# Kernel tuning notes

Hardware: AMD Instinct MI355X
Metric: run time of the kernel (lower is better)

Reference implementation:

```python
import jax, jax.numpy as jnp
import numpy as np

G, NPG, D_IN, HID, NH, DH = 128, 256, 15, 128, 8, 16
N = G * NPG
E = 1_048_576
NLAYERS = 3
EPS = 1e-5


def ln(x, g, b):
    m = x.mean(-1, keepdims=True)
    v = ((x - m) ** 2).mean(-1, keepdims=True)
    return (x - m) * jax.lax.rsqrt(v + EPS) * g + b


def gcn_conv(x, src, dst, W, b):
    # PyG GCNConv: add self-loops, symmetric deg^-1/2 normalization
    n = x.shape[0]
    h = x @ W  # [N, H]
    loop = jnp.arange(n)
    s = jnp.concatenate([src, loop])
    d = jnp.concatenate([dst, loop])
    deg = jnp.zeros((n,), x.dtype).at[d].add(1.0)  # >=1 due to self-loops
    dis = jax.lax.rsqrt(deg)
    coef = (dis[s] * dis[d])[:, None]
    return jnp.zeros_like(h).at[d].add(h[s] * coef) + b


def setup_inputs() -> dict:
    key = jax.random.key(0)
    ks = jax.random.split(key, 40)
    i = iter(range(40))

    def w(shape, scale=0.05):
        return jax.random.normal(ks[next(i)], shape, jnp.float32) * scale

    inp = {
        'x': jax.random.normal(ks[next(i)], (N, D_IN), jnp.float32),
        'edge_index': jax.random.randint(ks[next(i)], (2, E), 0, N),
        'batch': jnp.repeat(jnp.arange(G), NPG),  # 128 graphs x 256 nodes
        # input_proj: Linear + LayerNorm
        'W_in': w((D_IN, HID)), 'b_in': jnp.zeros((HID,)),
        'g_in': jnp.ones((HID,)), 'be_in': jnp.zeros((HID,)),
        # 3 GCNConv layers + LayerNorms (stacked)
        'Wc': w((NLAYERS, HID, HID)), 'bc': jnp.zeros((NLAYERS, HID)),
        'gn': jnp.ones((NLAYERS, HID)), 'bn': jnp.zeros((NLAYERS, HID)),
        # MultiheadAttention (in_proj split into q/k/v) + out_proj + post-LN
        'Wq': w((HID, HID)), 'bq': jnp.zeros((HID,)),
        'Wk': w((HID, HID)), 'bk': jnp.zeros((HID,)),
        'Wv': w((HID, HID)), 'bv': jnp.zeros((HID,)),
        'Wo': w((HID, HID)), 'bo': jnp.zeros((HID,)),
        'ga': jnp.ones((HID,)), 'ba': jnp.zeros((HID,)),
        # classifier: Linear(3H->H)+LN, Linear(H->H//2), Linear(H//2->2)
        'W1': w((3 * HID, HID)), 'b1': jnp.zeros((HID,)),
        'g1': jnp.ones((HID,)), 'beta1': jnp.zeros((HID,)),
        'W2': w((HID, HID // 2)), 'b2': jnp.zeros((HID // 2,)),
        'W3': w((HID // 2, 2)), 'b3': jnp.zeros((2,)),
    }
    return inp


def reference(x, edge_index, batch, W_in, b_in, g_in, be_in, Wc, bc, gn, bn,
              Wq, bq, Wk, bk, Wv, bv, Wo, bo, ga, ba,
              W1, b1, g1, beta1, W2, b2, W3, b3):
    src, dst = edge_index[0], edge_index[1]
    # input_proj (dropout is identity in eval)
    h = jax.nn.relu(ln(x @ W_in + b_in, g_in, be_in))
    # causal_graph_forward: GCN + LN + ReLU, residual for layers > 0
    for i in range(NLAYERS):
        h_res = h
        h = jax.nn.relu(ln(gcn_conv(h, src, dst, Wc[i], bc[i]), gn[i], bn[i]))
        if i > 0:
            h = h + h_res
    # per-graph MHA: equal-sized graphs -> block-diagonal == batched attention
    hg = h.reshape(G, NPG, HID)
    scale = 1.0 / np.sqrt(DH).astype(np.float32)
    q = (hg @ Wq.T + bq).reshape(G, NPG, NH, DH).transpose(0, 2, 1, 3)
    k = (hg @ Wk.T + bk).reshape(G, NPG, NH, DH).transpose(0, 2, 1, 3)
    v = (hg @ Wv.T + bv).reshape(G, NPG, NH, DH).transpose(0, 2, 1, 3)
    att = jax.nn.softmax(jnp.einsum('ghid,ghjd->ghij', q, k) * scale, axis=-1)
    o = jnp.einsum('ghij,ghjd->ghid', att, v).transpose(0, 2, 1, 3).reshape(G, NPG, HID)
    hg = ln(o @ Wo.T + bo + hg, ga, ba)
    # global mean/max/sum pooling per graph
    pooled = jnp.concatenate([hg.mean(1), hg.max(1), hg.sum(1)], axis=-1)  # [G, 3H]
    # classifier
    z = jax.nn.relu(ln(pooled @ W1 + b1, g1, beta1))
    z = jax.nn.relu(z @ W2 + b2)
    return z @ W3 + b3
```

## Files before the change

### kernel.cpp

```cpp
#include <hip/hip_runtime.h>
#include <hip/hip_bf16.h>

#define N_NODES 32768
#define E_EDGES 1048576
#define HID 128
#define G_GRAPHS 128
#define NPG 256
#define NH 8
#define DH 16
#define EPS 1e-5f
#define CHUNK 4096
#define BCAP 8192

typedef __attribute__((ext_vector_type(4))) float f32x4;
typedef __attribute__((ext_vector_type(4))) short bf16x4;

static __device__ __forceinline__ unsigned short bfbits(float f) {
    return __builtin_bit_cast(unsigned short, __float2bfloat16(f));
}
static __device__ __forceinline__ float bf2f(unsigned short u) {
    return __builtin_bit_cast(float, (unsigned)u << 16);
}
static __device__ __forceinline__ float rdlanef(float v, int l) {
    return __builtin_bit_cast(float, __builtin_amdgcn_readlane(__builtin_bit_cast(int, v), l));
}

__device__ __forceinline__ void ln_stats128(float v, float& mean, float& istd, float* red) {
    float s = v, s2 = v * v;
#pragma unroll
    for (int off = 32; off; off >>= 1) { s += __shfl_xor(s, off); s2 += __shfl_xor(s2, off); }
    int w = threadIdx.x >> 6;
    if ((threadIdx.x & 63) == 0) { red[w * 2] = s; red[w * 2 + 1] = s2; }
    __syncthreads();
    float ts = red[0] + red[2], ts2 = red[1] + red[3];
    mean = ts * (1.f / 128.f);
    float var = ts2 * (1.f / 128.f) - mean * mean;
    istd = rsqrtf(var + EPS);
    __syncthreads();
}

__global__ __launch_bounds__(256) void bucket_count(const int* __restrict__ dst,
                                                    int* __restrict__ bucket_cnt) {
    __shared__ int bcnt[256];
    int tid = threadIdx.x;
    bcnt[tid] = 0;
    __syncthreads();
    int base = blockIdx.x * CHUNK;
#pragma unroll
    for (int j = 0; j < 16; j++) {
        int d = dst[base + j * 256 + tid];
        atomicAdd(&bcnt[d >> 7], 1);
    }
    __syncthreads();
    atomicAdd(&bucket_cnt[tid], bcnt[tid]);
}

__global__ __launch_bounds__(256) void scan_buckets(const int* __restrict__ bucket_cnt,
                                                    int* __restrict__ bucket_base,
                                                    int* __restrict__ bucket_fill) {
    __shared__ int sc[256];
    int t = threadIdx.x;
    int c = bucket_cnt[t];
    sc[t] = c;
    __syncthreads();
    for (int off = 1; off < 256; off <<= 1) {
        int v = (t >= off) ? sc[t - off] : 0;
        __syncthreads();
        sc[t] += v;
        __syncthreads();
    }
    int ex = sc[t] - c;
    bucket_base[t] = ex;
    bucket_fill[t] = ex;
    if (t == 255) bucket_base[256] = sc[255];
}

__global__ __launch_bounds__(256) void bucket_scatter(const int* __restrict__ src,
                                                      const int* __restrict__ dst,
                                                      int* __restrict__ bucket_fill,
                                                      int* __restrict__ packed) {
    __shared__ int bcnt[256];
    __shared__ int lsc[256];
    __shared__ int delta[256];
    __shared__ int sorted[CHUNK];
    int tid = threadIdx.x;
    int base = blockIdx.x * CHUNK;
    int pk[16], bk[16], rk[16];
    bcnt[tid] = 0;
    __syncthreads();
#pragma unroll
    for (int j = 0; j < 16; j++) {
        int e = base + j * 256 + tid;
        int d = dst[e], s = src[e];
        pk[j] = (d << 15) | s;
        bk[j] = d >> 7;
    }
#pragma unroll
    for (int j = 0; j < 16; j++) rk[j] = atomicAdd(&bcnt[bk[j]], 1);
    __syncthreads();
    int cnt_t = bcnt[tid];
    lsc[tid] = cnt_t;
    __syncthreads();
    for (int off = 1; off < 256; off <<= 1) {
        int v = (tid >= off) ? lsc[tid - off] : 0;
        __syncthreads();
        lsc[tid] += v;
        __syncthreads();
    }
    int ls_t = lsc[tid] - cnt_t;
    __syncthreads();
    lsc[tid] = ls_t;
    int g = 0;
    if (cnt_t > 0) g = atomicAdd(&bucket_fill[tid], cnt_t);
    delta[tid] = g - ls_t;
    __syncthreads();
#pragma unroll
    for (int j = 0; j < 16; j++) sorted[lsc[bk[j]] + rk[j]] = pk[j];
    __syncthreads();
    for (int i = tid; i < CHUNK; i += 256) {
        int u = sorted[i];
        int b2 = u >> 22;
        packed[delta[b2] + i] = u;
    }
}

__global__ __launch_bounds__(256) void csr_build(const int* __restrict__ bucket_base,
                                                 const int* __restrict__ packed,
                                                 int* __restrict__ srcs,
                                                 int* __restrict__ row_ptr,
                                                 float* __restrict__ dis) {
    __shared__ int ncnt[128];
    __shared__ int sc[128];
    __shared__ int fill[128];
    __shared__ int outl[BCAP];
    int b = blockIdx.x, tid = threadIdx.x;
    int c0 = bucket_base[b], c1 = bucket_base[b + 1];
    int cnt = c1 - c0;
    if (tid < 128) ncnt[tid] = 0;
    __syncthreads();
    for (int i = tid; i < cnt; i += 256) {
        int u = packed[c0 + i];
        atomicAdd(&ncnt[(u >> 15) & 127], 1);
    }
    __syncthreads();
    int c = (tid < 128) ? ncnt[tid] : 0;
    if (tid < 128) sc[tid] = c;
    __syncthreads();
    for (int off = 1; off < 128; off <<= 1) {
        int v = (tid < 128 && tid >= off) ? sc[tid - off] : 0;
        __syncthreads();
        if (tid < 128) sc[tid] += v;
        __syncthreads();
    }
    if (tid < 128) {
        int ex = sc[tid] - c;
        fill[tid] = ex;
        int node = b * 128 + tid;
        row_ptr[node] = c0 + ex;
        dis[node] = rsqrtf((float)(c + 1));
    }
    if (b == 255 && tid == 0) row_ptr[N_NODES] = c1;
    __syncthreads();
    if (cnt <= BCAP) {
        for (int i = tid; i < cnt; i += 256) {
            int u = packed[c0 + i];
            int p = atomicAdd(&fill[(u >> 15) & 127], 1);
            outl[p] = u & 32767;
        }
        __syncthreads();
        for (int i = tid; i < cnt; i += 256) srcs[c0 + i] = outl[i];
    } else {
        for (int i = tid; i < cnt; i += 256) {
            int u = packed[c0 + i];
            int p = atomicAdd(&fill[(u >> 15) & 127], 1);
            srcs[c0 + p] = u & 32767;
        }
    }
}

__global__ __launch_bounds__(256) void prep_weights(const float* __restrict__ Wc,
                                                    const float* __restrict__ Wq,
                                                    const float* __restrict__ Wk,
                                                    const float* __restrict__ Wv,
                                                    const float* __restrict__ Wo,
                                                    const float* __restrict__ bq,
                                                    const float* __restrict__ bk,
                                                    const float* __restrict__ bv,
                                                    unsigned short* __restrict__ Wpk,
                                                    float* __restrict__ bT) {
    int m = blockIdx.y;
    int idx = blockIdx.x * 256 + threadIdx.x;
    int j = idx & 3, ln = (idx >> 2) & 63, kt = (idx >> 8) & 7, jt = (idx >> 11) & 7;
    int k = kt * 16 + (ln >> 4) * 4 + j;
    int col = jt * 16 + (ln & 15);
    float val;
    if (m < 3) val = Wc[m * 16384 + k * 128 + col];
    else {
        const float* W = (m == 3) ? Wq : (m == 4) ? Wk : (m == 5) ? Wv : Wo;
        val = W[col * 128 + k];
    }
    Wpk[m * 16384 + idx] = bfbits(val);
    if (m >= 3 && m < 6 && idx < 128) {
        const float* bs = (m == 3) ? bq : (m == 4) ? bk : bv;
        bT[(m - 3) * 128 + idx] = bs[idx];
    }
}

__global__ __launch_bounds__(128) void input_proj(const float* __restrict__ x,
                                                  const float* __restrict__ W,
                                                  const float* __restrict__ b,
                                                  const float* __restrict__ g,
                                                  const float* __restrict__ be,
                                                  unsigned short* __restrict__ h16) {
    int n = blockIdx.x, j = threadIdx.x;
    __shared__ float xs[15];
    __shared__ float red[4];
    if (j < 15) xs[j] = x[n * 15 + j];
    __syncthreads();
    float acc = b[j];
#pragma unroll
    for (int k = 0; k < 15; k++) acc += xs[k] * W[k * 128 + j];
    float m, is;
    ln_stats128(acc, m, is, red);
    float y = (acc - m) * is * g[j] + be[j];
    h16[(long)n * 128 + j] = bfbits(fmaxf(y, 0.f));
}

template <int MODE>
__device__ __forceinline__ void gemm_mfma_body(const unsigned short* __restrict__ in16,
                                               const unsigned short* __restrict__ Wpk,
                                               const float* __restrict__ bias,
                                               const unsigned short* __restrict__ resid16,
                                               const float* __restrict__ gamma,
                                               const float* __restrict__ beta,
                                               unsigned short* __restrict__ out16) {
    __shared__ unsigned short Ws[16384];
    __shared__ unsigned short Hs[64][136];
    int tid = threadIdx.x;
    long base = (long)blockIdx.x * 64;
    {
        const uint4* s4 = (const uint4*)Wpk;
        uint4* d4 = (uint4*)Ws;
        for (int i = tid; i < 2048; i += 256) d4[i] = s4[i];
        const unsigned short* hsrc = in16 + base * 128;
        for (int i = tid; i < 1024; i += 256) {
            int r = i >> 4, c8 = i & 15;
            *(uint4*)&Hs[r][c8 * 8] = *(const uint4*)&hsrc[r * 128 + c8 * 8];
        }
    }
    __syncthreads();
    int wv = tid >> 6, lane = tid & 63;
    int ql = lane & 15, qg = lane >> 4;
    f32x4 acc[8];
#pragma unroll
    for (int jt = 0; jt < 8; jt++) acc[jt] = (f32x4){0.f, 0.f, 0.f, 0.f};
#pragma unroll
    for (int kt = 0; kt < 8; kt++) {
        bf16x4 af = *(const bf16x4*)&Hs[wv * 16 + ql][kt * 16 + qg * 4];
#pragma unroll
        for (int jt = 0; jt < 8; jt++) {
            bf16x4 bf = *(const bf16x4*)&Ws[((jt * 8 + kt) * 64 + lane) * 4];
            acc[jt] = __builtin_amdgcn_mfma_f32_16x16x16bf16_1k(af, bf, acc[jt], 0, 0, 0);
        }
    }
    if (MODE >= 1) {
#pragma unroll
        for (int jt = 0; jt < 8; jt++) {
            float bv = bias[jt * 16 + ql];
#pragma unroll
            for (int r = 0; r < 4; r++) acc[jt][r] += bv;
        }
    }
    if (MODE == 2) {
#pragma unroll
        for (int jt = 0; jt < 8; jt++)
#pragma unroll
            for (int r = 0; r < 4; r++)
                acc[jt][r] += bf2f(resid16[(base + wv * 16 + qg * 4 + r) * 128 + jt * 16 + ql]);
        float s[4], s2[4], mean[4], istd[4];
#pragma unroll
        for (int r = 0; r < 4; r++) { s[r] = 0.f; s2[r] = 0.f; }
#pragma unroll
        for (int jt = 0; jt < 8; jt++)
#pragma unroll
            for (int r = 0; r < 4; r++) { float v = acc[jt][r]; s[r] += v; s2[r] += v * v; }
#pragma unroll
        for (int off = 1; off < 16; off <<= 1)
#pragma unroll
            for (int r = 0; r < 4; r++) {
                s[r] += __shfl_xor(s[r], off);
                s2[r] += __shfl_xor(s2[r], off);
            }
#pragma unroll
        for (int r = 0; r < 4; r++) {
            mean[r] = s[r] * (1.f / 128.f);
            float var = s2[r] * (1.f / 128.f) - mean[r] * mean[r];
            istd[r] = rsqrtf(var + EPS);
        }
#pragma unroll
        for (int jt = 0; jt < 8; jt++) {
            float gv = gamma[jt * 16 + ql], bev = beta[jt * 16 + ql];
#pragma unroll
            for (int r = 0; r < 4; r++)
                acc[jt][r] = (acc[jt][r] - mean[r]) * istd[r] * gv + bev;
        }
    }
#pragma unroll
    for (int jt = 0; jt < 8; jt++)
#pragma unroll
        for (int r = 0; r < 4; r++)
            Hs[wv * 16 + qg * 4 + r][jt * 16 + ql] = bfbits(acc[jt][r]);
#pragma unroll
    for (int p = 0; p < 4; p++) {
        int rl = p * 4 + qg;
        uint4 v = *(const uint4*)&Hs[wv * 16 + rl][ql * 8];
        *(uint4*)&out16[(base + wv * 16 + rl) * 128 + ql * 8] = v;
    }
}

template <int MODE>
__global__ __launch_bounds__(256) void gemm_mfma(const unsigned short* __restrict__ in16,
                                                 const unsigned short* __restrict__ Wpk,
                                                 const float* __restrict__ bias,
                                                 const unsigned short* __restrict__ resid16,
                                                 const float* __restrict__ gamma,
                                                 const float* __restrict__ beta,
                                                 unsigned short* __restrict__ out16) {
    gemm_mfma_body<MODE>(in16, Wpk, bias, resid16, gamma, beta, out16);
}

__global__ __launch_bounds__(256) void gemm_qkv(const unsigned short* __restrict__ in16,
                                                const unsigned short* __restrict__ Wpk,
                                                const float* __restrict__ bT,
                                                unsigned short* __restrict__ outb) {
    int y = blockIdx.y;
    gemm_mfma_body<1>(in16, Wpk + (3 + y) * 16384, bT + y * 128, nullptr, nullptr, nullptr,
                      outb + (long)y * N_NODES * 128);
}

__global__ __launch_bounds__(256) void gcn_agg(const unsigned short* __restrict__ hW,
                                               const int* __restrict__ row_ptr,
                                               const int* __restrict__ srcs,
                                               const float* __restrict__ dis,
                                               const float* __restrict__ bias,
                                               const float* __restrict__ gamma,
                                               const float* __restrict__ beta,
                                               unsigned short* __restrict__ h16, int with_resid) {
    int wv = threadIdx.x >> 6, lane = threadIdx.x & 63;
    int n = blockIdx.x * 4 + wv;
    int r0 = row_ptr[n], r1 = row_ptr[n + 1];
    float dn = dis[n];
    unsigned su = *(const unsigned*)&hW[(long)n * 128 + lane * 2];
    float dnn = dn * dn;
    float a0 = bf2f((unsigned short)(su & 0xffff)) * dnn;
    float a1 = bf2f((unsigned short)(su >> 16)) * dnn;
    for (int b = r0; b < r1; b += 64) {
        int cnt = min(64, r1 - b);
        int sv = n;
        float cv = 0.f;
        if (lane < cnt) {
            sv = srcs[b + lane];
            cv = dis[sv] * dn;
        }
        int cntR = (cnt + 15) & ~15;
        for (int j = 0; j < cntR; j += 16) {
            unsigned u[16];
#pragma unroll
            for (int t = 0; t < 16; t++) {
                int s = __builtin_amdgcn_readlane(sv, j + t);
                u[t] = *(const unsigned*)&hW[(long)s * 128 + lane * 2];
            }
#pragma unroll
            for (int t = 0; t < 16; t++) {
                float c = rdlanef(cv, j + t);
                a0 += bf2f((unsigned short)(u[t] & 0xffff)) * c;
                a1 += bf2f((unsigned short)(u[t] >> 16)) * c;
            }
        }
    }
    float2 bb = *(const float2*)&bias[lane * 2];
    a0 += bb.x;
    a1 += bb.y;
    float s = a0 + a1, s2 = a0 * a0 + a1 * a1;
#pragma unroll
    for (int off = 1; off < 64; off <<= 1) { s += __shfl_xor(s, off); s2 += __shfl_xor(s2, off); }
    float mean = s * (1.f / 128.f);
    float var = s2 * (1.f / 128.f) - mean * mean;
    float is = rsqrtf(var + EPS);
    float2 gg = *(const float2*)&gamma[lane * 2];
    float2 be2 = *(const float2*)&beta[lane * 2];
    float y0 = fmaxf((a0 - mean) * is * gg.x + be2.x, 0.f);
    float y1 = fmaxf((a1 - mean) * is * gg.y + be2.y, 0.f);
    if (with_resid) {
        unsigned ru = *(const unsigned*)&h16[(long)n * 128 + lane * 2];
        y0 += bf2f((unsigned short)(ru & 0xffff));
        y1 += bf2f((unsigned short)(ru >> 16));
    }
    unsigned outu = (unsigned)bfbits(y0) | ((unsigned)bfbits(y1) << 16);
    *(unsigned*)&h16[(long)n * 128 + lane * 2] = outu;
}

__global__ __launch_bounds__(256) void attention(const unsigned short* __restrict__ q16,
                                                 const unsigned short* __restrict__ k16,
                                                 const unsigned short* __restrict__ v16,
                                                 unsigned short* __restrict__ o16) {
    int g = blockIdx.x, hh = blockIdx.y;
    int tid = threadIdx.x;
    long gbase = ((long)g * NPG) * 128 + hh * 16;
    __shared__ unsigned short Ksh[256][24];
    __shared__ unsigned short Qsh[256][24];
    __shared__ unsigned short Vt[16][264];
    {
        const unsigned short* kp = k16 + gbase + (long)tid * 128;
        uint4 a = *(const uint4*)kp, b = *(const uint4*)(kp + 8);
        *(uint4*)&Ksh[tid][0] = a; *(uint4*)&Ksh[tid][8] = b;
        const unsigned short* qp = q16 + gbase + (long)tid * 128;
        uint4 c = *(const uint4*)qp, d = *(const uint4*)(qp + 8);
        *(uint4*)&Qsh[tid][0] = c; *(uint4*)&Qsh[tid][8] = d;
        const unsigned short* vp = v16 + gbase + (long)tid * 128;
#pragma unroll
        for (int dd = 0; dd < 16; dd++) Vt[dd][tid] = vp[dd];
    }
    __syncthreads();
    int wv = tid >> 6, lane = tid & 63;
    int qg = lane >> 4, ql = lane & 15;
    bf16x4 vfrag[16];
#pragma unroll
    for (int kt = 0; kt < 16; kt++)
        vfrag[kt] = *(const bf16x4*)&Vt[ql][kt * 16 + qg * 4];
    const float C = 0.36067376022224085f;
    for (int qi = 0; qi < 4; qi++) {
        int qt = wv * 4 + qi;
        bf16x4 qfrag = *(const bf16x4*)&Qsh[qt * 16 + ql][qg * 4];
        float lsum = 0.f;
        bf16x4 pb[16];
        f32x4 z4 = {0.f, 0.f, 0.f, 0.f};
#pragma unroll
        for (int kt = 0; kt < 16; kt++) {
            bf16x4 kfrag = *(const bf16x4*)&Ksh[kt * 16 + ql][qg * 4];
            f32x4 s4 = __builtin_amdgcn_mfma_f32_16x16x16bf16_1k(kfrag, qfrag, z4, 0, 0, 0);
            bf16x4 pbk;
#pragma unroll
            for (int r = 0; r < 4; r++) {
                float pv = exp2f(s4[r] * C);
                lsum += pv;
                pbk[r] = (short)bfbits(pv);
            }
            pb[kt] = pbk;
        }
        f32x4 oacc = {0.f, 0.f, 0.f, 0.f};
#pragma unroll
        for (int kt = 0; kt < 16; kt++)
            oacc = __builtin_amdgcn_mfma_f32_16x16x16bf16_1k(vfrag[kt], pb[kt], oacc, 0, 0, 0);
        lsum += __shfl_xor(lsum, 16);
        lsum += __shfl_xor(lsum, 32);
        float inv = 1.f / lsum;
        unsigned short* op = o16 + gbase + (long)(qt * 16 + ql) * 128 + 4 * qg;
        ushort4 st;
        st.x = bfbits(oacc[0] * inv);
        st.y = bfbits(oacc[1] * inv);
        st.z = bfbits(oacc[2] * inv);
        st.w = bfbits(oacc[3] * inv);
        *(ushort4*)op = st;
    }
}

__global__ __launch_bounds__(256) void pool_kernel(const unsigned short* __restrict__ hg,
                                                   float* __restrict__ pooled) {
    int g = blockIdx.x;
    int lane = threadIdx.x & 63, grp = threadIdx.x >> 6;
    __shared__ float ssum[4][128];
    __shared__ float smax[4][128];
    float s0 = 0.f, s1 = 0.f, m0 = -1e30f, m1 = -1e30f;
    for (int i = grp * 64; i < grp * 64 + 64; i++) {
        unsigned u = *(const unsigned*)&hg[((long)g * NPG + i) * 128 + lane * 2];
        float v0 = bf2f((unsigned short)(u & 0xffff));
        float v1 = bf2f((unsigned short)(u >> 16));
        s0 += v0; s1 += v1;
        m0 = fmaxf(m0, v0); m1 = fmaxf(m1, v1);
    }
    ssum[grp][lane * 2] = s0; ssum[grp][lane * 2 + 1] = s1;
    smax[grp][lane * 2] = m0; smax[grp][lane * 2 + 1] = m1;
    __syncthreads();
    if (grp == 0) {
        for (int jj = lane; jj < 128; jj += 64) {
            float ts = ssum[0][jj] + ssum[1][jj] + ssum[2][jj] + ssum[3][jj];
            float tm = fmaxf(fmaxf(smax[0][jj], smax[1][jj]), fmaxf(smax[2][jj], smax[3][jj]));
            pooled[g * 384 + jj] = ts * (1.f / 256.f);
            pooled[g * 384 + 128 + jj] = tm;
            pooled[g * 384 + 256 + jj] = ts;
        }
    }
}

__global__ __launch_bounds__(128) void classifier(const float* __restrict__ pooled,
                                                  const float* __restrict__ W1, const float* __restrict__ b1,
                                                  const float* __restrict__ g1, const float* __restrict__ be1,
                                                  const float* __restrict__ W2, const float* __restrict__ b2,
                                                  const float* __restrict__ W3, const float* __restrict__ b3,
                                                  float* __restrict__ out) {
    int g = blockIdx.x, j = threadIdx.x;
    __shared__ float pl[384];
    __shared__ float z1s[128];
    __shared__ float z2s[64];
    __shared__ float red[4];
    for (int i = j; i < 384; i += 128) pl[i] = pooled[g * 384 + i];
    __syncthreads();
    float acc = b1[j];
    for (int kk = 0; kk < 384; kk++) acc += pl[kk] * W1[kk * 128 + j];
    float m, is;
    ln_stats128(acc, m, is, red);
    float y = fmaxf((acc - m) * is * g1[j] + be1[j], 0.f);
    z1s[j] = y;
    __syncthreads();
    if (j < 64) {
        float a2 = b2[j];
        for (int kk = 0; kk < 128; kk++) a2 += z1s[kk] * W2[kk * 64 + j];
        z2s[j] = fmaxf(a2, 0.f);
    }
    __syncthreads();
    if (j < 64) {
        float vv = z2s[j];
        float p0 = vv * W3[j * 2];
        float p1 = vv * W3[j * 2 + 1];
#pragma unroll
        for (int off = 32; off; off >>= 1) { p0 += __shfl_xor(p0, off); p1 += __shfl_xor(p1, off); }
        if (j == 0) {
            out[g * 2] = p0 + b3[0];
            out[g * 2 + 1] = p1 + b3[1];
        }
    }
}

extern "C" void kernel_launch(void* const* d_in, const int* in_sizes, int n_in,
                              void* d_out, int out_size, void* d_ws, size_t ws_size,
                              hipStream_t stream) {
    const float* x = (const float*)d_in[0];
    const int* ei = (const int*)d_in[1];
    const float* W_in = (const float*)d_in[3];
    const float* b_in = (const float*)d_in[4];
    const float* g_in = (const float*)d_in[5];
    const float* be_in = (const float*)d_in[6];
    const float* Wc = (const float*)d_in[7];
    const float* bc = (const float*)d_in[8];
    const float* gn = (const float*)d_in[9];
    const float* bn = (const float*)d_in[10];
    const float* Wq = (const float*)d_in[11];
    const float* bq = (const float*)d_in[12];
    const float* Wk = (const float*)d_in[13];
    const float* bk = (const float*)d_in[14];
    const float* Wv = (const float*)d_in[15];
    const float* bv = (const float*)d_in[16];
    const float* Wo = (const float*)d_in[17];
    const float* bo = (const float*)d_in[18];
    const float* ga = (const float*)d_in[19];
    const float* ba = (const float*)d_in[20];
    const float* W1 = (const float*)d_in[21];
    const float* b1 = (const float*)d_in[22];
    const float* g1 = (const float*)d_in[23];
    const float* be1 = (const float*)d_in[24];
    const float* W2 = (const float*)d_in[25];
    const float* b2 = (const float*)d_in[26];
    const float* W3 = (const float*)d_in[27];
    const float* b3 = (const float*)d_in[28];
    float* out = (float*)d_out;

    const long NF = (long)N_NODES * 128;
    unsigned char* wsb = (unsigned char*)d_ws;
    const size_t MB = 1 << 20;
    unsigned short* h16 = (unsigned short*)(wsb);
    unsigned short* hw16 = (unsigned short*)(wsb + 8 * MB);
    unsigned short* qkv16 = (unsigned short*)(wsb + 16 * MB);
    unsigned short* o16 = (unsigned short*)(wsb + 40 * MB);
    unsigned short* hg16 = (unsigned short*)(wsb + 48 * MB);
    unsigned short* Wpk = (unsigned short*)(wsb + 56 * MB);
    int* packed = (int*)(wsb + 57 * MB);
    int* srcs = (int*)(wsb + 61 * MB);
    int* row_ptr = (int*)(wsb + 65 * MB);
    float* dis = (float*)(wsb + 66 * MB);
    float* bT = (float*)(wsb + 67 * MB);
    float* pooled = (float*)(wsb + 67 * MB + 4096);
    int* bucket_cnt = (int*)(wsb + 68 * MB);
    int* bucket_base = bucket_cnt + 256;
    int* bucket_fill = bucket_base + 257;

    const int* e_src = ei;
    const int* e_dst = ei + E_EDGES;

    hipMemsetAsync(bucket_cnt, 0, 256 * sizeof(int), stream);
    prep_weights<<<dim3(64, 7), 256, 0, stream>>>(Wc, Wq, Wk, Wv, Wo, bq, bk, bv, Wpk, bT);
    bucket_count<<<E_EDGES / CHUNK, 256, 0, stream>>>(e_dst, bucket_cnt);
    scan_buckets<<<1, 256, 0, stream>>>(bucket_cnt, bucket_base, bucket_fill);
    bucket_scatter<<<E_EDGES / CHUNK, 256, 0, stream>>>(e_src, e_dst, bucket_fill, packed);
    csr_build<<<256, 256, 0, stream>>>(bucket_base, packed, srcs, row_ptr, dis);

    input_proj<<<N_NODES, 128, 0, stream>>>(x, W_in, b_in, g_in, be_in, h16);

    for (int i = 0; i < 3; i++) {
        gemm_mfma<0><<<N_NODES / 64, 256, 0, stream>>>(h16, Wpk + i * 16384, nullptr, nullptr,
                                                       nullptr, nullptr, hw16);
        gcn_agg<<<N_NODES / 4, 256, 0, stream>>>(hw16, row_ptr, srcs, dis, bc + i * 128,
                                                 gn + i * 128, bn + i * 128, h16, i > 0);
    }

    gemm_qkv<<<dim3(N_NODES / 64, 3), 256, 0, stream>>>(h16, Wpk, bT, qkv16);

    attention<<<dim3(G_GRAPHS, NH), 256, 0, stream>>>(qkv16, qkv16 + NF, qkv16 + 2 * NF, o16);

    gemm_mfma<2><<<N_NODES / 64, 256, 0, stream>>>(o16, Wpk + 6 * 16384, bo, h16, ga, ba, hg16);

    pool_kernel<<<G_GRAPHS, 256, 0, stream>>>(hg16, pooled);
    classifier<<<G_GRAPHS, 128, 0, stream>>>(pooled, W1, b1, g1, be1, W2, b2, W3, b3, out);
}
```

Baseline: 367.0 us.

## Replace bucket count/scan pass with fixed-stride bucket slots in CSR build

Removes the separate bucket_count and scan_buckets kernels by giving each destination bucket a fixed-capacity region (BSTRIDE entries) so bucket_scatter can atomically claim offsets without a prior global count. csr_build reads per-bucket counts from bucket_fill and emits both row_ptr and row_end, since rows are no longer contiguous across buckets. This saves one full pass over dst and two launches, but assumes no bucket exceeds 16384 edges (expected around 4096 for uniform random edges) and uses more workspace.

```diff
diff --git a/kernel.cpp b/kernel.cpp
--- a/kernel.cpp
+++ b/kernel.cpp
@@ -11,6 +11,7 @@
 #define EPS 1e-5f
 #define CHUNK 4096
 #define BCAP 8192
+#define BSTRIDE 16384
 
 typedef __attribute__((ext_vector_type(4))) float f32x4;
 typedef __attribute__((ext_vector_type(4))) short bf16x4;
@@ -37,42 +38,6 @@
     float var = ts2 * (1.f / 128.f) - mean * mean;
     istd = rsqrtf(var + EPS);
     __syncthreads();
-}
-
-__global__ __launch_bounds__(256) void bucket_count(const int* __restrict__ dst,
-                                                    int* __restrict__ bucket_cnt) {
-    __shared__ int bcnt[256];
-    int tid = threadIdx.x;
-    bcnt[tid] = 0;
-    __syncthreads();
-    int base = blockIdx.x * CHUNK;
-#pragma unroll
-    for (int j = 0; j < 16; j++) {
-        int d = dst[base + j * 256 + tid];
-        atomicAdd(&bcnt[d >> 7], 1);
-    }
-    __syncthreads();
-    atomicAdd(&bucket_cnt[tid], bcnt[tid]);
-}
-
-__global__ __launch_bounds__(256) void scan_buckets(const int* __restrict__ bucket_cnt,
-                                                    int* __restrict__ bucket_base,
-                                                    int* __restrict__ bucket_fill) {
-    __shared__ int sc[256];
-    int t = threadIdx.x;
-    int c = bucket_cnt[t];
-    sc[t] = c;
-    __syncthreads();
-    for (int off = 1; off < 256; off <<= 1) {
-        int v = (t >= off) ? sc[t - off] : 0;
-        __syncthreads();
-        sc[t] += v;
-        __syncthreads();
-    }
-    int ex = sc[t] - c;
-    bucket_base[t] = ex;
-    bucket_fill[t] = ex;
-    if (t == 255) bucket_base[256] = sc[255];
 }
 
 __global__ __launch_bounds__(256) void bucket_scatter(const int* __restrict__ src,
@@ -112,7 +77,7 @@
     lsc[tid] = ls_t;
     int g = 0;
     if (cnt_t > 0) g = atomicAdd(&bucket_fill[tid], cnt_t);
-    delta[tid] = g - ls_t;
+    delta[tid] = tid * BSTRIDE + g - ls_t;
     __syncthreads();
 #pragma unroll
     for (int j = 0; j < 16; j++) sorted[lsc[bk[j]] + rk[j]] = pk[j];
@@ -124,18 +89,19 @@
     }
 }
 
-__global__ __launch_bounds__(256) void csr_build(const int* __restrict__ bucket_base,
+__global__ __launch_bounds__(256) void csr_build(const int* __restrict__ bucket_fill,
                                                  const int* __restrict__ packed,
                                                  int* __restrict__ srcs,
                                                  int* __restrict__ row_ptr,
+                                                 int* __restrict__ row_end,
                                                  float* __restrict__ dis) {
     __shared__ int ncnt[128];
     __shared__ int sc[128];
     __shared__ int fill[128];
     __shared__ int outl[BCAP];
     int b = blockIdx.x, tid = threadIdx.x;
-    int c0 = bucket_base[b], c1 = bucket_base[b + 1];
-    int cnt = c1 - c0;
+    int c0 = b * BSTRIDE;
+    int cnt = bucket_fill[b];
     if (tid < 128) ncnt[tid] = 0;
     __syncthreads();
     for (int i = tid; i < cnt; i += 256) {
@@ -157,9 +123,9 @@
         fill[tid] = ex;
         int node = b * 128 + tid;
         row_ptr[node] = c0 + ex;
+        row_end[node] = c0 + ex + c;
         dis[node] = rsqrtf((float)(c + 1));
     }
-    if (b == 255 && tid == 0) row_ptr[N_NODES] = c1;
     __syncthreads();
     if (cnt <= BCAP) {
         for (int i = tid; i < cnt; i += 256) {
@@ -340,6 +306,7 @@
 
 __global__ __launch_bounds__(256) void gcn_agg(const unsigned short* __restrict__ hW,
                                                const int* __restrict__ row_ptr,
+                                               const int* __restrict__ row_end,
                                                const int* __restrict__ srcs,
                                                const float* __restrict__ dis,
                                                const float* __restrict__ bias,
@@ -348,7 +315,7 @@
                                                unsigned short* __restrict__ h16, int with_resid) {
     int wv = threadIdx.x >> 6, lane = threadIdx.x & 63;
     int n = blockIdx.x * 4 + wv;
-    int r0 = row_ptr[n], r1 = row_ptr[n + 1];
+    int r0 = row_ptr[n], r1 = row_end[n];
     float dn = dis[n];
     unsigned su = *(const unsigned*)&hW[(long)n * 128 + lane * 2];
     float dnn = dn * dn;
@@ -574,32 +541,29 @@
     unsigned short* o16 = (unsigned short*)(wsb + 40 * MB);
     unsigned short* hg16 = (unsigned short*)(wsb + 48 * MB);
     unsigned short* Wpk = (unsigned short*)(wsb + 56 * MB);
-    int* packed = (int*)(wsb + 57 * MB);
-    int* srcs = (int*)(wsb + 61 * MB);
-    int* row_ptr = (int*)(wsb + 65 * MB);
-    float* dis = (float*)(wsb + 66 * MB);
-    float* bT = (float*)(wsb + 67 * MB);
-    float* pooled = (float*)(wsb + 67 * MB + 4096);
-    int* bucket_cnt = (int*)(wsb + 68 * MB);
-    int* bucket_base = bucket_cnt + 256;
-    int* bucket_fill = bucket_base + 257;
+    int* srcs = (int*)(wsb + 57 * MB);
+    int* packed = (int*)(wsb + 73 * MB);
+    int* row_ptr = (int*)(wsb + 89 * MB);
+    int* row_end = (int*)(wsb + 90 * MB);
+    float* dis = (float*)(wsb + 91 * MB);
+    float* bT = (float*)(wsb + 92 * MB);
+    float* pooled = (float*)(wsb + 92 * MB + 4096);
+    int* bucket_fill = (int*)(wsb + 93 * MB);
 
     const int* e_src = ei;
     const int* e_dst = ei + E_EDGES;
 
-    hipMemsetAsync(bucket_cnt, 0, 256 * sizeof(int), stream);
+    hipMemsetAsync(bucket_fill, 0, 256 * sizeof(int), stream);
     prep_weights<<<dim3(64, 7), 256, 0, stream>>>(Wc, Wq, Wk, Wv, Wo, bq, bk, bv, Wpk, bT);
-    bucket_count<<<E_EDGES / CHUNK, 256, 0, stream>>>(e_dst, bucket_cnt);
-    scan_buckets<<<1, 256, 0, stream>>>(bucket_cnt, bucket_base, bucket_fill);
     bucket_scatter<<<E_EDGES / CHUNK, 256, 0, stream>>>(e_src, e_dst, bucket_fill, packed);
-    csr_build<<<256, 256, 0, stream>>>(bucket_base, packed, srcs, row_ptr, dis);
+    csr_build<<<256, 256, 0, stream>>>(bucket_fill, packed, srcs, row_ptr, row_end, dis);
 
     input_proj<<<N_NODES, 128, 0, stream>>>(x, W_in, b_in, g_in, be_in, h16);
 
     for (int i = 0; i < 3; i++) {
         gemm_mfma<0><<<N_NODES / 64, 256, 0, stream>>>(h16, Wpk + i * 16384, nullptr, nullptr,
                                                        nullptr, nullptr, hw16);
-        gcn_agg<<<N_NODES / 4, 256, 0, stream>>>(hw16, row_ptr, srcs, dis, bc + i * 128,
+        gcn_agg<<<N_NODES / 4, 256, 0, stream>>>(hw16, row_ptr, row_end, srcs, dis, bc + i * 128,
                                                  gn + i * 128, bn + i * 128, h16, i > 0);
     }
 
```

After: 352.6 us. 3.9% less time.
